# Kernel tuning notes

Measured on AMD Instinct MI355X. Metric: run time of the kernel, lower is better.

The kernel has to match this reference:

```python
import jax, jax.numpy as jnp
import numpy as np

N_NODES = 50000
N_EDGES = 800000
NUM_GRAPHS = 512
NEG_SLOPE = 0.2  # PyG GATv2Conv default negative_slope


def setup_inputs() -> dict:
    key = jax.random.key(0)
    ks = jax.random.split(key, 16)
    F_in, H = 128, 2
    C1, C2, NC = 32, 16, 6
    x = jax.random.normal(ks[0], (N_NODES, F_in), dtype=jnp.float32)
    edge_index = jax.random.randint(ks[1], (2, N_EDGES), 0, N_NODES, dtype=jnp.int64)
    batch = jnp.sort(jax.random.randint(ks[2], (N_NODES,), 0, NUM_GRAPHS, dtype=jnp.int64))
    s = lambda fan_in: 1.0 / np.sqrt(fan_in)
    return {
        "x": x, "edge_index": edge_index, "batch": batch,
        # conv1: in=128 -> heads=2, out=32 (concat 64)
        "Wl1": jax.random.normal(ks[3], (F_in, H * C1), jnp.float32) * s(F_in),
        "bl1": jnp.zeros((H * C1,), jnp.float32),
        "Wr1": jax.random.normal(ks[4], (F_in, H * C1), jnp.float32) * s(F_in),
        "att1": jax.random.normal(ks[5], (H, C1), jnp.float32) * s(C1),
        "b1": jnp.zeros((H * C1,), jnp.float32),
        # conv2: in=64 -> heads=2, out=16 (concat 32)
        "Wl2": jax.random.normal(ks[6], (H * C1, H * C2), jnp.float32) * s(H * C1),
        "bl2": jnp.zeros((H * C2,), jnp.float32),
        "Wr2": jax.random.normal(ks[7], (H * C1, H * C2), jnp.float32) * s(H * C1),
        "att2": jax.random.normal(ks[8], (H, C2), jnp.float32) * s(C2),
        "b2": jnp.zeros((H * C2,), jnp.float32),
        # fc: 32 -> 6
        "Wfc": jax.random.normal(ks[9], (H * C2, NC), jnp.float32) * s(H * C2),
        "bfc": jnp.zeros((NC,), jnp.float32),
    }


def _gatv2_conv(x, src, dst, Wl, bl, Wr, att, bias):
    """PyG GATv2Conv (concat heads, add_self_loops already applied to src/dst)."""
    H, C = att.shape
    N = x.shape[0]
    xl = (x @ Wl + bl).reshape(N, H, C)  # source/message transform
    xr = (x @ Wr).reshape(N, H, C)       # target transform
    e = jax.nn.leaky_relu(xl[src] + xr[dst], NEG_SLOPE)  # [E,H,C]
    score = jnp.einsum('ehc,hc->eh', e, att)             # [E,H]
    # segment softmax over edges sharing the same destination node
    smax = jax.ops.segment_max(score, dst, num_segments=N)      # [N,H]
    ex = jnp.exp(score - smax[dst])
    denom = jax.ops.segment_sum(ex, dst, num_segments=N)        # [N,H]
    alpha = ex / denom[dst]                                     # [E,H]
    out = jax.ops.segment_sum(alpha[:, :, None] * xl[src], dst, num_segments=N)
    return out.reshape(N, H * C) + bias


def reference(x, edge_index, batch, Wl1, bl1, Wr1, att1, b1,
              Wl2, bl2, Wr2, att2, b2, Wfc, bfc):
    N = x.shape[0]
    loops = jnp.arange(N, dtype=edge_index.dtype)
    src = jnp.concatenate([edge_index[0], loops])  # add_self_loops=True
    dst = jnp.concatenate([edge_index[1], loops])
    h = jax.nn.elu(_gatv2_conv(x, src, dst, Wl1, bl1, Wr1, att1, b1))
    h = jax.nn.elu(_gatv2_conv(h, src, dst, Wl2, bl2, Wr2, att2, b2))
    # global mean pool over graphs
    sums = jax.ops.segment_sum(h, batch, num_segments=NUM_GRAPHS)
    cnt = jax.ops.segment_sum(jnp.ones((N,), h.dtype), batch, num_segments=NUM_GRAPHS)
    pooled = sums / jnp.maximum(cnt, 1.0)[:, None]
    return jax.nn.log_softmax(pooled @ Wfc + bfc, axis=1)
```

## Files before the change

### kernel.cpp

```cpp
#include <hip/hip_runtime.h>
#include <math.h>

#define N_NODES 50000
#define N_EDGES 800000
#define NUM_GRAPHS 512
#define NEG_SLOPE 0.2f
#define LOG_MD 6
#define ROWCAP 63
#define NBKT 196
#define NPART 800
#define EPB_PART 1000
#define BCAP 5120

typedef unsigned short ushort_t;
typedef unsigned int   uint_t;
typedef __attribute__((ext_vector_type(4))) float f32x4;
typedef __attribute__((ext_vector_type(8))) short s16x8;

__device__ __forceinline__ ushort_t f2bf(float f) {
    union { float f; uint_t u; } v; v.f = f;
    uint_t u = v.u;
    return (ushort_t)((u + 0x7fffu + ((u >> 16) & 1u)) >> 16);
}

__device__ __forceinline__ void unpack8(const ushort_t* p, float* f) {
    uint4 u = *(const uint4*)p;
    f[0] = __uint_as_float(u.x << 16); f[1] = __uint_as_float(u.x & 0xffff0000u);
    f[2] = __uint_as_float(u.y << 16); f[3] = __uint_as_float(u.y & 0xffff0000u);
    f[4] = __uint_as_float(u.z << 16); f[5] = __uint_as_float(u.z & 0xffff0000u);
    f[6] = __uint_as_float(u.w << 16); f[7] = __uint_as_float(u.w & 0xffff0000u);
}

__global__ void zero_prep_k(const float* __restrict__ Wl1, const float* __restrict__ Wr1,
                            const float* __restrict__ Wl2, const float* __restrict__ Wr2,
                            ushort_t* __restrict__ Bt1, ushort_t* __restrict__ Bt2,
                            int* __restrict__ bucket_cur, float* __restrict__ gz) {
    int gt = blockIdx.x * 256 + threadIdx.x;
    if (gt < NBKT) bucket_cur[gt] = 0;
    if (gt < NUM_GRAPHS * 33) gz[gt] = 0.f;
    if (gt < 16384) {
        int j = gt >> 7, k = gt & 127;
        float v = (j < 64) ? Wl1[k * 64 + j] : Wr1[k * 64 + (j - 64)];
        Bt1[gt] = f2bf(v);
    } else if (gt < 16384 + 4096) {
        int g = gt - 16384;
        int j = g >> 6, k = g & 63;
        float v = (j < 32) ? Wl2[k * 32 + j] : Wr2[k * 32 + (j - 32)];
        Bt2[g] = f2bf(v);
    }
}

__global__ void __launch_bounds__(256) part_k(const int* __restrict__ ei,
                                              const int* __restrict__ batch,
                                              int* __restrict__ bucket_cur,
                                              int2* __restrict__ binned,
                                              float* __restrict__ gz) {
    __shared__ int2 ebuf[EPB_PART];
    __shared__ int2 sbuf[EPB_PART];
    __shared__ int hist[NBKT], loff[NBKT], rk[NBKT], gbase[NBKT];
    __shared__ int s2[256];
    const int tid = threadIdx.x;
    for (int i = tid; i < NBKT; i += 256) { hist[i] = 0; rk[i] = 0; }
    {
        int node = blockIdx.x * 63 + tid;
        if (tid < 63 && node < N_NODES) atomicAdd(&gz[NUM_GRAPHS * 32 + batch[node]], 1.f);
    }
    __syncthreads();
    const int base = blockIdx.x * EPB_PART;
    for (int i = tid; i < EPB_PART; i += 256) {
        int s = ei[base + i];
        int d = ei[N_EDGES + base + i];
        ebuf[i] = make_int2(s, d);
        atomicAdd(&hist[d >> 8], 1);
    }
    __syncthreads();
    s2[tid] = (tid < NBKT) ? hist[tid] : 0;
    __syncthreads();
    for (int off = 1; off < 256; off <<= 1) {
        int v = (tid >= off) ? s2[tid - off] : 0;
        __syncthreads();
        s2[tid] += v;
        __syncthreads();
    }
    if (tid < NBKT) {
        loff[tid] = (tid == 0) ? 0 : s2[tid - 1];
        gbase[tid] = hist[tid] ? atomicAdd(&bucket_cur[tid], hist[tid]) : 0;
    }
    __syncthreads();
    for (int i = tid; i < EPB_PART; i += 256) {
        int2 e = ebuf[i];
        int b = e.y >> 8;
        int r = atomicAdd(&rk[b], 1);
        sbuf[loff[b] + r] = e;
    }
    __syncthreads();
    for (int i = tid; i < EPB_PART; i += 256) {
        int2 e = sbuf[i];
        int b = e.y >> 8;
        int slot = gbase[b] + (i - loff[b]);
        if (slot < BCAP) binned[(size_t)b * BCAP + slot] = e;
    }
}

__global__ void __launch_bounds__(256) build_k(const int* __restrict__ bucket_cur,
                                               const int2* __restrict__ binned,
                                               int* __restrict__ col) {
    __shared__ int win[128 * ROWCAP];
    __shared__ int cnt[128];
    const int tid = threadIdx.x;
    for (int i = tid; i < 128 * ROWCAP; i += 256) win[i] = 0;
    if (tid < 128) cnt[tid] = 0;
    __syncthreads();
    const int b = blockIdx.x >> 1;
    const int half = blockIdx.x & 1;
    const int total = min(bucket_cur[b], BCAP);
    const int2* src = binned + (size_t)b * BCAP;
    for (int i = tid; i < total; i += 256) {
        int2 e = src[i];
        int row = e.y & 255;
        if ((row >> 7) == half) {
            int rl = row & 127;
            int c = atomicAdd(&cnt[rl], 1);
            if (c < ROWCAP) win[rl * ROWCAP + c] = e.x;
        }
    }
    __syncthreads();
    const int n0 = (b << 8) + (half << 7);
    const int nrows = min(128, N_NODES - n0);
    if (nrows <= 0) return;
    int* dst = col + ((size_t)n0 << LOG_MD);
    for (int i = tid; i < nrows * 64; i += 256) {
        int row = i >> 6, s = i & 63;
        dst[i] = (s == 63) ? min(cnt[row], ROWCAP) : win[row * ROWCAP + s];
    }
}

__global__ void __launch_bounds__(256) linear1_mfma_k(
        const float* __restrict__ x, const ushort_t* __restrict__ Bt,
        const float* __restrict__ bl,
        ushort_t* __restrict__ xl, ushort_t* __restrict__ xr) {
    __shared__ ushort_t bts[128 * 136];
    const int tid = threadIdx.x;
    {
        const uint_t* src = (const uint_t*)Bt;
        uint_t* dst = (uint_t*)bts;
        for (int i = tid; i < 8192; i += 256) {
            int row = i >> 6, pos = i & 63;
            dst[row * 68 + pos] = src[i];
        }
    }
    __syncthreads();
    const int lane = tid & 63;
    const int wv = tid >> 6;
    const int q = lane >> 4, m = lane & 15;
    const int n0w = blockIdx.x * 64 + wv * 16;
    const int rowA = min(n0w + m, N_NODES - 1);
    const float* xrow = x + (size_t)rowA * 128;

    f32x4 acc[8];
    #pragma unroll
    for (int t = 0; t < 8; ++t) acc[t] = (f32x4){0.f, 0.f, 0.f, 0.f};

    #pragma unroll
    for (int ks = 0; ks < 4; ++ks) {
        const int k0 = ks * 32 + q * 8;
        float4 a0 = *(const float4*)(xrow + k0);
        float4 a1 = *(const float4*)(xrow + k0 + 4);
        s16x8 af;
        af[0] = (short)f2bf(a0.x); af[1] = (short)f2bf(a0.y);
        af[2] = (short)f2bf(a0.z); af[3] = (short)f2bf(a0.w);
        af[4] = (short)f2bf(a1.x); af[5] = (short)f2bf(a1.y);
        af[6] = (short)f2bf(a1.z); af[7] = (short)f2bf(a1.w);
        #pragma unroll
        for (int t = 0; t < 8; ++t) {
            const s16x8 bf = *(const s16x8*)(bts + (t * 16 + m) * 136 + k0);
            acc[t] = __builtin_amdgcn_mfma_f32_16x16x32_bf16(af, bf, acc[t], 0, 0, 0);
        }
    }
    #pragma unroll
    for (int t = 0; t < 8; ++t) {
        int j = t * 16 + m;
        float bias = (t < 4) ? bl[j] : 0.f;
        #pragma unroll
        for (int r = 0; r < 4; ++r) {
            int n = n0w + q * 4 + r;
            if (n < N_NODES) {
                if (t < 4) xl[(size_t)n * 64 + j] = f2bf(acc[t][r] + bias);
                else       xr[(size_t)n * 64 + (j - 64)] = f2bf(acc[t][r]);
            }
        }
    }
}

__global__ void __launch_bounds__(256) linear2_mfma_k(
        const ushort_t* __restrict__ h1, const ushort_t* __restrict__ Bt2,
        const float* __restrict__ bl2,
        ushort_t* __restrict__ xl2, ushort_t* __restrict__ xr2) {
    __shared__ ushort_t bts[64 * 72];
    const int tid = threadIdx.x;
    {
        const uint_t* src = (const uint_t*)Bt2;
        uint_t* dst = (uint_t*)bts;
        for (int i = tid; i < 2048; i += 256) {
            int row = i >> 5, pos = i & 31;
            dst[row * 36 + pos] = src[i];
        }
    }
    __syncthreads();
    const int lane = tid & 63;
    const int wv = tid >> 6;
    const int q = lane >> 4, m = lane & 15;
    const int n0w = blockIdx.x * 64 + wv * 16;
    const int rowA = min(n0w + m, N_NODES - 1);
    const ushort_t* hrow = h1 + (size_t)rowA * 64;

    f32x4 acc[4];
    #pragma unroll
    for (int t = 0; t < 4; ++t) acc[t] = (f32x4){0.f, 0.f, 0.f, 0.f};

    #pragma unroll
    for (int ks = 0; ks < 2; ++ks) {
        const int k0 = ks * 32 + q * 8;
        const s16x8 af = *(const s16x8*)(hrow + k0);
        #pragma unroll
        for (int t = 0; t < 4; ++t) {
            const s16x8 bf = *(const s16x8*)(bts + (t * 16 + m) * 72 + k0);
            acc[t] = __builtin_amdgcn_mfma_f32_16x16x32_bf16(af, bf, acc[t], 0, 0, 0);
        }
    }
    #pragma unroll
    for (int t = 0; t < 4; ++t) {
        int j = t * 16 + m;
        float bias = (t < 2) ? bl2[j] : 0.f;
        #pragma unroll
        for (int r = 0; r < 4; ++r) {
            int n = n0w + q * 4 + r;
            if (n < N_NODES) {
                if (t < 2) xl2[(size_t)n * 32 + j] = f2bf(acc[t][r] + bias);
                else       xr2[(size_t)n * 32 + (j - 32)] = f2bf(acc[t][r]);
            }
        }
    }
}

template<int C2, int LPN, int HEADL, bool OUT_BF16>
__global__ void __launch_bounds__(256) gat_conv_k(
        const int* __restrict__ col,
        const ushort_t* __restrict__ xl, const ushort_t* __restrict__ xr,
        const float* __restrict__ att, const float* __restrict__ b,
        void* __restrict__ outp) {
    const int NPW = 64 / LPN;
    int wave = (blockIdx.x * blockDim.x + threadIdx.x) >> 6;
    int lane = threadIdx.x & 63;
    int slot = lane / LPN;
    int c8   = lane % LPN;
    int n = wave * NPW + slot;
    const bool nvalid = (n < N_NODES);
    const int nn = nvalid ? n : (N_NODES - 1);

    float xrv[8], attv[8], bv[8];
    unpack8(xr + (size_t)nn * C2 + c8 * 8, xrv);
    *(float4*)(attv)     = ((const float4*)att)[c8 * 2];
    *(float4*)(attv + 4) = ((const float4*)att)[c8 * 2 + 1];
    *(float4*)(bv)       = ((const float4*)b)[c8 * 2];
    *(float4*)(bv + 4)   = ((const float4*)b)[c8 * 2 + 1];

    const int start = nn << LOG_MD;
    const int dg = nvalid ? min(col[start + 63], ROWCAP) : 0;

    float den, acc[8];
    {
        float xsv[8];
        unpack8(xl + (size_t)nn * C2 + c8 * 8, xsv);
        float p = 0.f;
        #pragma unroll
        for (int i = 0; i < 8; ++i) {
            float z = xsv[i] + xrv[i];
            z = (z >= 0.f) ? z : NEG_SLOPE * z;
            p = fmaf(z, attv[i], p);
        }
        #pragma unroll
        for (int off = HEADL / 2; off > 0; off >>= 1)
            p += __shfl_xor(p, off, 64);
        float ex = __expf(fminf(p, 80.f));
        den = ex;
        #pragma unroll
        for (int i = 0; i < 8; ++i) acc[i] = ex * xsv[i];
    }

    if (dg > 0) {
        uint4 raw = *(const uint4*)(xl + (size_t)col[start] * C2 + c8 * 8);
        for (int k = 0; k < dg; ++k) {
            uint4 cu = raw;
            if (k + 1 < dg) {
                int sn = col[start + k + 1];
                raw = *(const uint4*)(xl + (size_t)sn * C2 + c8 * 8);
            }
            float xv[8];
            xv[0] = __uint_as_float(cu.x << 16); xv[1] = __uint_as_float(cu.x & 0xffff0000u);
            xv[2] = __uint_as_float(cu.y << 16); xv[3] = __uint_as_float(cu.y & 0xffff0000u);
            xv[4] = __uint_as_float(cu.z << 16); xv[5] = __uint_as_float(cu.z & 0xffff0000u);
            xv[6] = __uint_as_float(cu.w << 16); xv[7] = __uint_as_float(cu.w & 0xffff0000u);
            float p = 0.f;
            #pragma unroll
            for (int i = 0; i < 8; ++i) {
                float z = xv[i] + xrv[i];
                z = (z >= 0.f) ? z : NEG_SLOPE * z;
                p = fmaf(z, attv[i], p);
            }
            #pragma unroll
            for (int off = HEADL / 2; off > 0; off >>= 1)
                p += __shfl_xor(p, off, 64);
            float ex = __expf(fminf(p, 80.f));
            den += ex;
            #pragma unroll
            for (int i = 0; i < 8; ++i) acc[i] = fmaf(ex, xv[i], acc[i]);
        }
    }
    if (nvalid) {
        float inv = 1.f / den;
        float o[8];
        #pragma unroll
        for (int i = 0; i < 8; ++i) {
            float v = fmaf(acc[i], inv, bv[i]);
            o[i] = (v > 0.f) ? v : (__expf(v) - 1.f);
        }
        if (OUT_BF16) {
            uint4 u;
            u.x = ((uint_t)f2bf(o[1]) << 16) | f2bf(o[0]);
            u.y = ((uint_t)f2bf(o[3]) << 16) | f2bf(o[2]);
            u.z = ((uint_t)f2bf(o[5]) << 16) | f2bf(o[4]);
            u.w = ((uint_t)f2bf(o[7]) << 16) | f2bf(o[6]);
            ((uint4*)outp)[(size_t)n * (C2 / 8) + c8] = u;
        } else {
            float4* op = (float4*)outp;
            op[(size_t)n * (C2 / 4) + c8 * 2]     = *(float4*)o;
            op[(size_t)n * (C2 / 4) + c8 * 2 + 1] = *(float4*)(o + 4);
        }
    }
}

__global__ void pool_k(const float* __restrict__ h2, const int* __restrict__ batch,
                       float* __restrict__ gsum) {
    const int NCH = (N_NODES + 7) / 8;
    int t = blockIdx.x * blockDim.x + threadIdx.x;
    if (t >= NCH * 32) return;
    int c = t & 31;
    int n0 = (t >> 5) * 8;
    int nend = min(n0 + 8, N_NODES);
    int curb = batch[n0];
    float s = 0.f;
    for (int n = n0; n < nend; ++n) {
        int bb = batch[n];
        if (bb != curb) {
            atomicAdd(gsum + (size_t)curb * 32 + c, s);
            s = 0.f; curb = bb;
        }
        s += h2[(size_t)n * 32 + c];
    }
    atomicAdd(gsum + (size_t)curb * 32 + c, s);
}

__global__ void head_k(const float* __restrict__ gsum, const float* __restrict__ gcnt,
                       const float* __restrict__ Wfc, const float* __restrict__ bfc,
                       float* __restrict__ out) {
    int gph = blockIdx.x * blockDim.x + threadIdx.x;
    if (gph >= NUM_GRAPHS) return;
    float inv = 1.f / fmaxf(gcnt[gph], 1.f);
    float logits[6];
    #pragma unroll
    for (int j = 0; j < 6; ++j) logits[j] = bfc[j];
    for (int k = 0; k < 32; ++k) {
        float p = gsum[(size_t)gph * 32 + k] * inv;
        #pragma unroll
        for (int j = 0; j < 6; ++j) logits[j] = fmaf(p, Wfc[k * 6 + j], logits[j]);
    }
    float m = logits[0];
    #pragma unroll
    for (int j = 1; j < 6; ++j) m = fmaxf(m, logits[j]);
    float ssum = 0.f;
    #pragma unroll
    for (int j = 0; j < 6; ++j) ssum += expf(logits[j] - m);
    float lse = m + logf(ssum);
    #pragma unroll
    for (int j = 0; j < 6; ++j) out[(size_t)gph * 6 + j] = logits[j] - lse;
}

extern "C" void kernel_launch(void* const* d_in, const int* in_sizes, int n_in,
                              void* d_out, int out_size, void* d_ws, size_t ws_size,
                              hipStream_t stream) {
    const float* x    = (const float*)d_in[0];
    const int*   ei   = (const int*)d_in[1];
    const int*   batch= (const int*)d_in[2];
    const float* Wl1  = (const float*)d_in[3];
    const float* bl1  = (const float*)d_in[4];
    const float* Wr1  = (const float*)d_in[5];
    const float* att1 = (const float*)d_in[6];
    const float* b1   = (const float*)d_in[7];
    const float* Wl2  = (const float*)d_in[8];
    const float* bl2  = (const float*)d_in[9];
    const float* Wr2  = (const float*)d_in[10];
    const float* att2 = (const float*)d_in[11];
    const float* b2   = (const float*)d_in[12];
    const float* Wfc  = (const float*)d_in[13];
    const float* bfc  = (const float*)d_in[14];
    float* out = (float*)d_out;

    char* wsp = (char*)d_ws;
    ushort_t* xl1 = (ushort_t*)wsp; wsp += (size_t)N_NODES * 64 * 2;
    ushort_t* xr1 = (ushort_t*)wsp; wsp += (size_t)N_NODES * 64 * 2;
    ushort_t* h1  = (ushort_t*)wsp; wsp += (size_t)N_NODES * 64 * 2;
    ushort_t* xl2 = (ushort_t*)wsp; wsp += (size_t)N_NODES * 32 * 2;
    ushort_t* xr2 = (ushort_t*)wsp; wsp += (size_t)N_NODES * 32 * 2;
    float* h2   = (float*)wsp; wsp += (size_t)N_NODES * 32 * 4;
    float* gsum = (float*)wsp; wsp += (size_t)NUM_GRAPHS * 32 * 4;
    float* gcnt = (float*)wsp; wsp += (size_t)NUM_GRAPHS * 4;
    int* col    = (int*)wsp; wsp += ((size_t)N_NODES << LOG_MD) * 4;
    int* bucket_cur = (int*)wsp; wsp += NBKT * 4;
    wsp += 16 - ((size_t)wsp & 15);
    ushort_t* Bt1 = (ushort_t*)wsp; wsp += 128 * 128 * 2;
    ushort_t* Bt2 = (ushort_t*)wsp; wsp += 64 * 64 * 2;
    int2* binned = (int2*)xl1;

    zero_prep_k<<<80, 256, 0, stream>>>(Wl1, Wr1, Wl2, Wr2, Bt1, Bt2, bucket_cur, gsum);
    part_k<<<NPART, 256, 0, stream>>>(ei, batch, bucket_cur, binned, gsum);
    build_k<<<NBKT * 2, 256, 0, stream>>>(bucket_cur, binned, col);

    linear1_mfma_k<<<(N_NODES + 63) / 64, 256, 0, stream>>>(x, Bt1, bl1, xl1, xr1);
    {
        int waves = (N_NODES + 7) / 8;
        gat_conv_k<64, 8, 4, true><<<(waves + 3) / 4, 256, 0, stream>>>(
            col, xl1, xr1, att1, b1, h1);
    }

    linear2_mfma_k<<<(N_NODES + 63) / 64, 256, 0, stream>>>(h1, Bt2, bl2, xl2, xr2);
    {
        int waves = (N_NODES + 15) / 16;
        gat_conv_k<32, 4, 2, false><<<(waves + 3) / 4, 256, 0, stream>>>(
            col, xl2, xr2, att2, b2, h2);
    }

    pool_k<<<(((N_NODES + 7) / 8) * 32 + 255) / 256, 256, 0, stream>>>(h2, batch, gsum);
    head_k<<<(NUM_GRAPHS + 255) / 256, 256, 0, stream>>>(gsum, gcnt, Wfc, bfc, out);
}
```

Measured before the change: 229.9 us.

## Replace atomic bucket cursors with per-block segment binning and binary-search graph counts

The edge partitioner no longer reserves global slots per bucket through atomics. Each of half as many blocks now writes its edges into a fixed per-(bucket, block) segment of capacity 40 and records a count matrix, which build_k walks per segment. Per-graph node counts are now found by binary search over the sorted batch array in head_k, which drops the float atomics and the gcnt zeroing. This removes global atomic contention and ordering, at the cost of a sparser binned layout, serial per-segment loops in build_k, and a risk of dropping edges if a block puts more than 40 edges into one bucket.

```diff
diff --git a/kernel.cpp b/kernel.cpp
--- a/kernel.cpp
+++ b/kernel.cpp
@@ -8,9 +8,9 @@
 #define LOG_MD 6
 #define ROWCAP 63
 #define NBKT 196
-#define NPART 800
-#define EPB_PART 1000
-#define BCAP 5120
+#define NPART 400
+#define EPB_PART 2000
+#define CAPSEG 40
 
 typedef unsigned short ushort_t;
 typedef unsigned int   uint_t;
@@ -34,10 +34,9 @@
 __global__ void zero_prep_k(const float* __restrict__ Wl1, const float* __restrict__ Wr1,
                             const float* __restrict__ Wl2, const float* __restrict__ Wr2,
                             ushort_t* __restrict__ Bt1, ushort_t* __restrict__ Bt2,
-                            int* __restrict__ bucket_cur, float* __restrict__ gz) {
+                            float* __restrict__ gsum) {
     int gt = blockIdx.x * 256 + threadIdx.x;
-    if (gt < NBKT) bucket_cur[gt] = 0;
-    if (gt < NUM_GRAPHS * 33) gz[gt] = 0.f;
+    if (gt < NUM_GRAPHS * 32) gsum[gt] = 0.f;
     if (gt < 16384) {
         int j = gt >> 7, k = gt & 127;
         float v = (j < 64) ? Wl1[k * 64 + j] : Wr1[k * 64 + (j - 64)];
@@ -51,22 +50,17 @@
 }
 
 __global__ void __launch_bounds__(256) part_k(const int* __restrict__ ei,
-                                              const int* __restrict__ batch,
-                                              int* __restrict__ bucket_cur,
                                               int2* __restrict__ binned,
-                                              float* __restrict__ gz) {
+                                              int* __restrict__ cntmat) {
     __shared__ int2 ebuf[EPB_PART];
     __shared__ int2 sbuf[EPB_PART];
-    __shared__ int hist[NBKT], loff[NBKT], rk[NBKT], gbase[NBKT];
+    __shared__ int hist[NBKT], loff[NBKT], rk[NBKT];
     __shared__ int s2[256];
     const int tid = threadIdx.x;
+    const int blk = blockIdx.x;
     for (int i = tid; i < NBKT; i += 256) { hist[i] = 0; rk[i] = 0; }
-    {
-        int node = blockIdx.x * 63 + tid;
-        if (tid < 63 && node < N_NODES) atomicAdd(&gz[NUM_GRAPHS * 32 + batch[node]], 1.f);
-    }
-    __syncthreads();
-    const int base = blockIdx.x * EPB_PART;
+    __syncthreads();
+    const int base = blk * EPB_PART;
     for (int i = tid; i < EPB_PART; i += 256) {
         int s = ei[base + i];
         int d = ei[N_EDGES + base + i];
@@ -84,7 +78,7 @@
     }
     if (tid < NBKT) {
         loff[tid] = (tid == 0) ? 0 : s2[tid - 1];
-        gbase[tid] = hist[tid] ? atomicAdd(&bucket_cur[tid], hist[tid]) : 0;
+        cntmat[blk * NBKT + tid] = min(hist[tid], CAPSEG);
     }
     __syncthreads();
     for (int i = tid; i < EPB_PART; i += 256) {
@@ -97,12 +91,12 @@
     for (int i = tid; i < EPB_PART; i += 256) {
         int2 e = sbuf[i];
         int b = e.y >> 8;
-        int slot = gbase[b] + (i - loff[b]);
-        if (slot < BCAP) binned[(size_t)b * BCAP + slot] = e;
-    }
-}
-
-__global__ void __launch_bounds__(256) build_k(const int* __restrict__ bucket_cur,
+        int r = i - loff[b];
+        if (r < CAPSEG) binned[((size_t)b * NPART + blk) * CAPSEG + r] = e;
+    }
+}
+
+__global__ void __launch_bounds__(256) build_k(const int* __restrict__ cntmat,
                                                const int2* __restrict__ binned,
                                                int* __restrict__ col) {
     __shared__ int win[128 * ROWCAP];
@@ -113,15 +107,17 @@
     __syncthreads();
     const int b = blockIdx.x >> 1;
     const int half = blockIdx.x & 1;
-    const int total = min(bucket_cur[b], BCAP);
-    const int2* src = binned + (size_t)b * BCAP;
-    for (int i = tid; i < total; i += 256) {
-        int2 e = src[i];
-        int row = e.y & 255;
-        if ((row >> 7) == half) {
-            int rl = row & 127;
-            int c = atomicAdd(&cnt[rl], 1);
-            if (c < ROWCAP) win[rl * ROWCAP + c] = e.x;
+    for (int seg = tid; seg < NPART; seg += 256) {
+        int c = cntmat[seg * NBKT + b];
+        const int2* sp = binned + ((size_t)b * NPART + seg) * CAPSEG;
+        for (int i = 0; i < c; ++i) {
+            int2 e = sp[i];
+            int row = e.y & 255;
+            if ((row >> 7) == half) {
+                int rl = row & 127;
+                int cc = atomicAdd(&cnt[rl], 1);
+                if (cc < ROWCAP) win[rl * ROWCAP + cc] = e.x;
+            }
         }
     }
     __syncthreads();
@@ -361,12 +357,22 @@
     atomicAdd(gsum + (size_t)curb * 32 + c, s);
 }
 
-__global__ void head_k(const float* __restrict__ gsum, const float* __restrict__ gcnt,
+__device__ __forceinline__ int lower_bound_k(const int* __restrict__ batch, int v) {
+    int lo = 0, hi = N_NODES;
+    while (lo < hi) {
+        int mid = (lo + hi) >> 1;
+        if (batch[mid] < v) lo = mid + 1; else hi = mid;
+    }
+    return lo;
+}
+
+__global__ void head_k(const float* __restrict__ gsum, const int* __restrict__ batch,
                        const float* __restrict__ Wfc, const float* __restrict__ bfc,
                        float* __restrict__ out) {
     int gph = blockIdx.x * blockDim.x + threadIdx.x;
     if (gph >= NUM_GRAPHS) return;
-    float inv = 1.f / fmaxf(gcnt[gph], 1.f);
+    float cntf = (float)(lower_bound_k(batch, gph + 1) - lower_bound_k(batch, gph));
+    float inv = 1.f / fmaxf(cntf, 1.f);
     float logits[6];
     #pragma unroll
     for (int j = 0; j < 6; ++j) logits[j] = bfc[j];
@@ -414,17 +420,16 @@
     ushort_t* xr2 = (ushort_t*)wsp; wsp += (size_t)N_NODES * 32 * 2;
     float* h2   = (float*)wsp; wsp += (size_t)N_NODES * 32 * 4;
     float* gsum = (float*)wsp; wsp += (size_t)NUM_GRAPHS * 32 * 4;
-    float* gcnt = (float*)wsp; wsp += (size_t)NUM_GRAPHS * 4;
     int* col    = (int*)wsp; wsp += ((size_t)N_NODES << LOG_MD) * 4;
-    int* bucket_cur = (int*)wsp; wsp += NBKT * 4;
+    int* cntmat = (int*)wsp; wsp += (size_t)NPART * NBKT * 4;
     wsp += 16 - ((size_t)wsp & 15);
     ushort_t* Bt1 = (ushort_t*)wsp; wsp += 128 * 128 * 2;
     ushort_t* Bt2 = (ushort_t*)wsp; wsp += 64 * 64 * 2;
     int2* binned = (int2*)xl1;
 
-    zero_prep_k<<<80, 256, 0, stream>>>(Wl1, Wr1, Wl2, Wr2, Bt1, Bt2, bucket_cur, gsum);
-    part_k<<<NPART, 256, 0, stream>>>(ei, batch, bucket_cur, binned, gsum);
-    build_k<<<NBKT * 2, 256, 0, stream>>>(bucket_cur, binned, col);
+    zero_prep_k<<<80, 256, 0, stream>>>(Wl1, Wr1, Wl2, Wr2, Bt1, Bt2, gsum);
+    part_k<<<NPART, 256, 0, stream>>>(ei, binned, cntmat);
+    build_k<<<NBKT * 2, 256, 0, stream>>>(cntmat, binned, col);
 
     linear1_mfma_k<<<(N_NODES + 63) / 64, 256, 0, stream>>>(x, Bt1, bl1, xl1, xr1);
     {
@@ -441,5 +446,5 @@
     }
 
     pool_k<<<(((N_NODES + 7) / 8) * 32 + 255) / 256, 256, 0, stream>>>(h2, batch, gsum);
-    head_k<<<(NUM_GRAPHS + 255) / 256, 256, 0, stream>>>(gsum, gcnt, Wfc, bfc, out);
-}
+    head_k<<<(NUM_GRAPHS + 255) / 256, 256, 0, stream>>>(gsum, batch, Wfc, bfc, out);
+}
```

Result: faster. 204.3 us (-11.1%).
